# Optimization experiments

Hardware: AMD Instinct MI355X
Metric: run time of the kernel (lower is better)

Reference implementation:

```python
import jax, jax.numpy as jnp
import numpy as np

B, T, D = 2, 4096, 768
H = 12
HD = D // H  # 64
SCALE = 1.0 / np.sqrt(HD)


def setup_inputs() -> dict:
    key = jax.random.key(0)
    k1, k2, k3 = jax.random.split(key, 3)
    x = jax.random.normal(k1, (B, T, D), dtype=jnp.float32)
    W_qkv = jax.random.normal(k2, (D, 3 * D), dtype=jnp.float32) * (1.0 / np.sqrt(D))
    b_qkv = jnp.zeros((3 * D,), dtype=jnp.float32)
    W_out = jax.random.normal(k3, (D, D), dtype=jnp.float32) * (1.0 / np.sqrt(D))
    b_out = jnp.zeros((D,), dtype=jnp.float32)
    return {"x": x, "W_qkv": W_qkv, "b_qkv": b_qkv, "W_out": W_out, "b_out": b_out}


def reference(x, W_qkv, b_qkv, W_out, b_out):
    Bx, Tx, C = x.shape
    qkv = x @ W_qkv + b_qkv                                  # [B,T,3D]
    qkv = qkv.reshape(Bx, Tx, 3, H, HD).transpose(2, 0, 3, 1, 4)  # [3,B,H,T,hd]
    q, k, v = qkv[0], qkv[1], qkv[2]
    scores = jnp.einsum('bhqd,bhkd->bhqk', q, k) * SCALE      # [B,H,T,T]
    causal = jnp.tril(jnp.ones((Tx, Tx), dtype=bool))
    scores = jnp.where(causal[None, None], scores, -jnp.inf)
    attn = jax.nn.softmax(scores, axis=-1)
    out = jnp.einsum('bhqk,bhkd->bhqd', attn, v)              # [B,H,T,hd]
    out = out.transpose(0, 2, 1, 3).reshape(Bx, Tx, C)        # [B,T,D]
    return out @ W_out + b_out
```

## Files before the change

### kernel.cpp

```cpp
#include <hip/hip_runtime.h>
#include <cstdint>
#include <cstddef>

typedef _Float16 f16x8 __attribute__((ext_vector_type(8)));
typedef _Float16 f16x4 __attribute__((ext_vector_type(4)));
typedef float    f32x4 __attribute__((ext_vector_type(4)));

#define AS_GLOBAL __attribute__((address_space(1)))
#define AS_LDS    __attribute__((address_space(3)))

__device__ __forceinline__ void load16_to_lds(const _Float16* g, _Float16* l) {
    __builtin_amdgcn_global_load_lds((const AS_GLOBAL void*)g, (AS_LDS void*)l, 16, 0, 0);
}

#define BB   2
#define TT   4096
#define DD   768
#define NH   12
#define HDIM 64
#define D3   2304
#define SC2  (0.125f * 1.44269504088896f)

__global__ void cast_f32_f16(const float* __restrict__ in, _Float16* __restrict__ out, int n) {
    int i = (blockIdx.x * blockDim.x + threadIdx.x) * 4;
    float4 v = *(const float4*)(in + i);
    f16x4 h;
    h[0] = (_Float16)v.x; h[1] = (_Float16)v.y;
    h[2] = (_Float16)v.z; h[3] = (_Float16)v.w;
    *(f16x4*)(out + i) = h;
}

__global__ void transpose_cast(const float* __restrict__ in, _Float16* __restrict__ out,
                               int R, int C) {
    __shared__ float tile[32][33];
    const int bx = blockIdx.x * 32, by = blockIdx.y * 32;
    const int tx = threadIdx.x, ty = threadIdx.y;
#pragma unroll
    for (int j = 0; j < 32; j += 8)
        tile[ty + j][tx] = in[(size_t)(by + ty + j) * C + bx + tx];
    __syncthreads();
#pragma unroll
    for (int j = 0; j < 32; j += 8)
        out[(size_t)(bx + ty + j) * R + by + tx] = (_Float16)tile[tx][ty + j];
}

template <typename OutT, bool BIAS_ROW>
__global__ __launch_bounds__(256) void gemm_bt(const _Float16* __restrict__ A,
                                               const _Float16* __restrict__ Bt,
                                               const float* __restrict__ bias,
                                               OutT* __restrict__ C,
                                               int M, int N, int K) {
    __shared__ __align__(16) _Float16 As[128 * 32];
    __shared__ __align__(16) _Float16 Bs[128 * 32];
    const int tid  = threadIdx.x;
    const int wave = tid >> 6, lane = tid & 63, quad = lane >> 4, l16 = lane & 15;
    const int m0 = blockIdx.y * 128, n0 = blockIdx.x * 128;
    const int wm = (wave & 1) * 64, wn = (wave >> 1) * 64;
    const int rowc = lane >> 2, part = lane & 3;

    f32x4 acc[4][4];
#pragma unroll
    for (int i = 0; i < 4; ++i)
#pragma unroll
        for (int n = 0; n < 4; ++n) acc[i][n] = f32x4{0.f, 0.f, 0.f, 0.f};

    for (int k0 = 0; k0 < K; k0 += 32) {
        __syncthreads();
#pragma unroll
        for (int cc = 0; cc < 2; ++cc) {
            const int ch = wave * 2 + cc;
            load16_to_lds(A  + (size_t)(m0 + ch * 16 + rowc) * K + k0 + part * 8,
                          As + ch * 512);
            load16_to_lds(Bt + (size_t)(n0 + ch * 16 + rowc) * K + k0 + part * 8,
                          Bs + ch * 512);
        }
        __syncthreads();
#pragma unroll
        for (int i = 0; i < 4; ++i) {
            f16x8 a = *(const f16x8*)(As + (wm + i * 16 + l16) * 32 + quad * 8);
#pragma unroll
            for (int n = 0; n < 4; ++n) {
                f16x8 b = *(const f16x8*)(Bs + (wn + n * 16 + l16) * 32 + quad * 8);
                acc[i][n] = __builtin_amdgcn_mfma_f32_16x16x32_f16(a, b, acc[i][n], 0, 0, 0);
            }
        }
    }
#pragma unroll
    for (int i = 0; i < 4; ++i)
#pragma unroll
        for (int n = 0; n < 4; ++n)
#pragma unroll
            for (int r = 0; r < 4; ++r) {
                const int row = m0 + wm + i * 16 + quad * 4 + r;
                const int col = n0 + wn + n * 16 + l16;
                const float bv = BIAS_ROW ? bias[row] : bias[col];
                C[(size_t)row * N + col] = (OutT)(acc[i][n][r] + bv);
            }
}

__global__ __launch_bounds__(256) void attn_kernel(const _Float16* __restrict__ qk,
                                                   const _Float16* __restrict__ vt,
                                                   _Float16* __restrict__ ao) {
    __shared__ __align__(16) _Float16 Ks[2][64 * 64];
    __shared__ __align__(16) _Float16 Vs[2][80 * 64];
    __shared__ __align__(16) _Float16 Ps[4][16 * 80];
    const int b = blockIdx.z, h = blockIdx.y;
    const int tid = threadIdx.x;
    const int wave = tid >> 6, lane = tid & 63, quad = lane >> 4, l16 = lane & 15;

    if (tid < 16) {
        f16x8 ones;
#pragma unroll
        for (int j = 0; j < 8; ++j) ones[j] = (_Float16)1.0f;
        *(f16x8*)(Vs[tid >> 3] + 64 * 64 + (tid & 7) * 8) = ones;
    }

    const _Float16* pK[2];
    const _Float16* pV[2];
#pragma unroll
    for (int p = 0; p < 2; ++p) {
        const int j  = wave * 16 + p * 8 + (lane >> 3);
        const int sig = (j & 15) * 4 + (j >> 4);
        const int cdk = (lane & 7) ^ (j & 7);
        pK[p] = qk + (size_t)(b * TT + sig) * 1536 + DD + h * HDIM + cdk * 8;
        pV[p] = vt + (size_t)(h * HDIM + j) * 8192 + b * TT + cdk * 8;
    }
    auto stage = [&](int buf, int k0) {
#pragma unroll
        for (int p = 0; p < 2; ++p) {
            load16_to_lds(pK[p] + (size_t)k0 * 1536, Ks[buf] + (wave * 16 + p * 8) * 64);
            load16_to_lds(pV[p] + k0,                Vs[buf] + (wave * 16 + p * 8) * 64);
        }
    };

    _Float16* pw[4];
#pragma unroll
    for (int r = 0; r < 4; ++r) {
        const int row = quad * 4 + r;
        pw[r] = Ps[wave] + row * 80 + (((l16 >> 1) ^ (row & 7)) * 8) + (l16 & 1) * 4;
    }
    const _Float16* pr[2];
#pragma unroll
    for (int kh = 0; kh < 2; ++kh)
        pr[kh] = Ps[wave] + l16 * 80 + (((kh * 4 + quad) ^ (l16 & 7)) * 8);

    auto process = [&](int qt) {
        const int q0 = qt * 64;
        const int nkt = qt + 1;
        const int qrow = q0 + wave * 16 + quad * 4;
        f16x8 aq[2];
        {
            const int q = q0 + wave * 16 + l16;
            const _Float16* qp = qk + (size_t)(b * TT + q) * 1536 + h * HDIM + quad * 8;
            const _Float16 sc = (_Float16)SC2;
            aq[0] = *(const f16x8*)qp * sc;
            aq[1] = *(const f16x8*)(qp + 32) * sc;
        }
        f32x4 o[5];
#pragma unroll
        for (int n = 0; n < 5; ++n) o[n] = f32x4{0.f, 0.f, 0.f, 0.f};

        __syncthreads();
        stage(0, 0);
        int cur = 0;
        for (int kt = 0; kt < nkt; ++kt) {
            __syncthreads();
            if (kt + 1 < nkt) stage(cur ^ 1, (kt + 1) * 64);

            f32x4 s[4];
#pragma unroll
            for (int n = 0; n < 4; ++n) s[n] = f32x4{0.f, 0.f, 0.f, 0.f};
#pragma unroll
            for (int kh = 0; kh < 2; ++kh)
#pragma unroll
                for (int n = 0; n < 4; ++n) {
                    const int pos = (kh * 4 + quad) ^ (l16 & 7);
                    f16x8 bk = *(const f16x8*)(Ks[cur] + (n * 16 + l16) * 64 + pos * 8);
                    s[n] = __builtin_amdgcn_mfma_f32_16x16x32_f16(aq[kh], bk, s[n], 0, 0, 0);
                }

            if (kt == nkt - 1) {
#pragma unroll
                for (int n = 0; n < 4; ++n) {
                    const int kg = kt * 64 + l16 * 4 + n;
#pragma unroll
                    for (int r = 0; r < 4; ++r)
                        if (kg > qrow + r) s[n][r] = -1e30f;
                }
            }

#pragma unroll
            for (int r = 0; r < 4; ++r) {
                f16x4 pk;
#pragma unroll
                for (int n = 0; n < 4; ++n)
                    pk[n] = (_Float16)__builtin_amdgcn_exp2f(s[n][r]);
                *(f16x4*)pw[r] = pk;
            }

#pragma unroll
            for (int kh = 0; kh < 2; ++kh) {
                f16x8 ap = *(const f16x8*)pr[kh];
#pragma unroll
                for (int n = 0; n < 5; ++n) {
                    const int posv = (kh * 4 + quad) ^ (l16 & 7);
                    f16x8 bv = *(const f16x8*)(Vs[cur] + (n * 16 + l16) * 64 + posv * 8);
                    o[n] = __builtin_amdgcn_mfma_f32_16x16x32_f16(ap, bv, o[n], 0, 0, 0);
                }
            }
            cur ^= 1;
        }

#pragma unroll
        for (int r = 0; r < 4; ++r) {
            const float lr = __shfl(o[4][r], lane & 48);
            const float inv = 1.0f / lr;
            const int q = qrow + r;
#pragma unroll
            for (int n = 0; n < 4; ++n) {
                const int col = h * HDIM + n * 16 + l16;
                ao[(size_t)(b * TT + q) * DD + col] = (_Float16)(o[n][r] * inv);
            }
        }
    };

    process(63 - blockIdx.x);
    process(blockIdx.x);
}

extern "C" void kernel_launch(void* const* d_in, const int* in_sizes, int n_in,
                              void* d_out, int out_size, void* d_ws, size_t ws_size,
                              hipStream_t stream) {
    const float* x     = (const float*)d_in[0];
    const float* Wqkv  = (const float*)d_in[1];
    const float* bqkv  = (const float*)d_in[2];
    const float* Wout  = (const float*)d_in[3];
    const float* bout  = (const float*)d_in[4];
    float* out = (float*)d_out;

    char* ws = (char*)d_ws;
    _Float16* Xh    = (_Float16*)ws;  ws += (size_t)BB * TT * DD * 2;
    _Float16* Wqkvt = (_Float16*)ws;  ws += (size_t)D3 * DD * 2;
    _Float16* Wot   = (_Float16*)ws;  ws += (size_t)DD * DD * 2;
    _Float16* QKh   = (_Float16*)ws;  ws += (size_t)BB * TT * 1536 * 2;
    _Float16* VtG   = (_Float16*)ws;  ws += (size_t)DD * BB * TT * 2;
    _Float16* AOh   = (_Float16*)ws;  ws += (size_t)BB * TT * DD * 2;

    const int M = BB * TT;

    cast_f32_f16<<<(M * DD) / (256 * 4), 256, 0, stream>>>(x, Xh, M * DD);
    transpose_cast<<<dim3(D3 / 32, DD / 32), dim3(32, 8), 0, stream>>>(Wqkv, Wqkvt, DD, D3);
    transpose_cast<<<dim3(DD / 32, DD / 32), dim3(32, 8), 0, stream>>>(Wout, Wot, DD, DD);

    gemm_bt<_Float16, false><<<dim3(1536 / 128, M / 128), 256, 0, stream>>>(
        Xh, Wqkvt, bqkv, QKh, M, 1536, DD);
    gemm_bt<_Float16, true><<<dim3(M / 128, DD / 128), 256, 0, stream>>>(
        Wqkvt + (size_t)1536 * DD, Xh, bqkv + 1536, VtG, DD, M, DD);

    attn_kernel<<<dim3(32, NH, BB), 256, 0, stream>>>(QKh, VtG, AOh);

    gemm_bt<float, false><<<dim3(DD / 128, M / 128), 256, 0, stream>>>(
        AOh, Wot, bout, out, M, DD, DD);
}
```

Before: 260.3 us.

## Merge prep and QKV GEMM launches; restructure attention to 2 waves × 32 rows

The three cast/transpose kernels are merged into one prep launch, and the QK and V projection GEMMs become a single launch, which cuts launch overhead and lets the two GEMMs share the GPU. The attention kernel now runs 128 threads, with each wave owning 32 query rows. Each loaded K/V fragment feeds two MFMAs, raising reuse. The row sum is now taken by a separate MFMA against a ones vector instead of a padded V column. Risks are higher register pressure and fewer waves per block to hide latency.

```diff
diff --git a/kernel.cpp b/kernel.cpp
--- a/kernel.cpp
+++ b/kernel.cpp
@@ -21,20 +21,35 @@
 #define D3   2304
 #define SC2  (0.125f * 1.44269504088896f)
 
-__global__ void cast_f32_f16(const float* __restrict__ in, _Float16* __restrict__ out, int n) {
-    int i = (blockIdx.x * blockDim.x + threadIdx.x) * 4;
-    float4 v = *(const float4*)(in + i);
-    f16x4 h;
-    h[0] = (_Float16)v.x; h[1] = (_Float16)v.y;
-    h[2] = (_Float16)v.z; h[3] = (_Float16)v.w;
-    *(f16x4*)(out + i) = h;
-}
-
-__global__ void transpose_cast(const float* __restrict__ in, _Float16* __restrict__ out,
-                               int R, int C) {
+__global__ __launch_bounds__(256) void prep(const float* __restrict__ x,
+                                            _Float16* __restrict__ Xh,
+                                            const float* __restrict__ Wqkv,
+                                            _Float16* __restrict__ Wqkvt,
+                                            const float* __restrict__ Wout,
+                                            _Float16* __restrict__ Wot) {
+    const int bid = blockIdx.x, tid = threadIdx.x;
+    if (bid < 6144) {
+        const int i = bid * 1024 + tid * 4;
+        float4 v = *(const float4*)(x + i);
+        f16x4 h;
+        h[0] = (_Float16)v.x; h[1] = (_Float16)v.y;
+        h[2] = (_Float16)v.z; h[3] = (_Float16)v.w;
+        *(f16x4*)(Xh + i) = h;
+        return;
+    }
     __shared__ float tile[32][33];
-    const int bx = blockIdx.x * 32, by = blockIdx.y * 32;
-    const int tx = threadIdx.x, ty = threadIdx.y;
+    const float* in; _Float16* out; int C, bx, by;
+    if (bid < 7872) {
+        const int t = bid - 6144;
+        in = Wqkv; out = Wqkvt; C = 2304;
+        bx = (t % 72) * 32; by = (t / 72) * 32;
+    } else {
+        const int t = bid - 7872;
+        in = Wout; out = Wot; C = 768;
+        bx = (t % 24) * 32; by = (t / 24) * 32;
+    }
+    const int R = 768;
+    const int tx = tid & 31, ty = tid >> 5;
 #pragma unroll
     for (int j = 0; j < 32; j += 8)
         tile[ty + j][tx] = in[(size_t)(by + ty + j) * C + bx + tx];
@@ -44,17 +59,15 @@
         out[(size_t)(bx + ty + j) * R + by + tx] = (_Float16)tile[tx][ty + j];
 }
 
-template <typename OutT, bool BIAS_ROW>
-__global__ __launch_bounds__(256) void gemm_bt(const _Float16* __restrict__ A,
-                                               const _Float16* __restrict__ Bt,
-                                               const float* __restrict__ bias,
-                                               OutT* __restrict__ C,
-                                               int M, int N, int K) {
-    __shared__ __align__(16) _Float16 As[128 * 32];
-    __shared__ __align__(16) _Float16 Bs[128 * 32];
+template <typename OutT>
+__device__ __forceinline__ void gemm_body(const _Float16* __restrict__ A,
+                                          const _Float16* __restrict__ Bt,
+                                          const float* __restrict__ bias, bool bias_row,
+                                          OutT* __restrict__ C, int N, int K,
+                                          int m0, int n0,
+                                          _Float16* As, _Float16* Bs) {
     const int tid  = threadIdx.x;
     const int wave = tid >> 6, lane = tid & 63, quad = lane >> 4, l16 = lane & 15;
-    const int m0 = blockIdx.y * 128, n0 = blockIdx.x * 128;
     const int wm = (wave & 1) * 64, wn = (wave >> 1) * 64;
     const int rowc = lane >> 2, part = lane & 3;
 
@@ -93,33 +106,60 @@
             for (int r = 0; r < 4; ++r) {
                 const int row = m0 + wm + i * 16 + quad * 4 + r;
                 const int col = n0 + wn + n * 16 + l16;
-                const float bv = BIAS_ROW ? bias[row] : bias[col];
+                const float bv = bias_row ? bias[row] : bias[col];
                 C[(size_t)row * N + col] = (OutT)(acc[i][n][r] + bv);
             }
 }
 
-__global__ __launch_bounds__(256) void attn_kernel(const _Float16* __restrict__ qk,
+__global__ __launch_bounds__(256) void gemm_qkv(const _Float16* __restrict__ Xh,
+                                                const _Float16* __restrict__ Wqkvt,
+                                                const float* __restrict__ bqkv,
+                                                _Float16* __restrict__ QKh,
+                                                _Float16* __restrict__ VtG) {
+    __shared__ __align__(16) _Float16 As[128 * 32];
+    __shared__ __align__(16) _Float16 Bs[128 * 32];
+    const int bid = blockIdx.x;
+    if (bid < 768) {
+        const int bx = bid % 12, by = bid / 12;
+        gemm_body<_Float16>(Xh, Wqkvt, bqkv, false, QKh, 1536, DD,
+                            by * 128, bx * 128, As, Bs);
+    } else {
+        const int t = bid - 768;
+        const int bx = t % 64, by = t / 64;
+        gemm_body<_Float16>(Wqkvt + (size_t)1536 * DD, Xh, bqkv + 1536, true, VtG,
+                            8192, DD, by * 128, bx * 128, As, Bs);
+    }
+}
+
+__global__ __launch_bounds__(256) void gemm_out(const _Float16* __restrict__ A,
+                                                const _Float16* __restrict__ Bt,
+                                                const float* __restrict__ bias,
+                                                float* __restrict__ C) {
+    __shared__ __align__(16) _Float16 As[128 * 32];
+    __shared__ __align__(16) _Float16 Bs[128 * 32];
+    gemm_body<float>(A, Bt, bias, false, C, DD, DD,
+                     (int)blockIdx.y * 128, (int)blockIdx.x * 128, As, Bs);
+}
+
+__global__ __launch_bounds__(128) void attn_kernel(const _Float16* __restrict__ qk,
                                                    const _Float16* __restrict__ vt,
                                                    _Float16* __restrict__ ao) {
     __shared__ __align__(16) _Float16 Ks[2][64 * 64];
-    __shared__ __align__(16) _Float16 Vs[2][80 * 64];
-    __shared__ __align__(16) _Float16 Ps[4][16 * 80];
+    __shared__ __align__(16) _Float16 Vs[2][64 * 64];
+    __shared__ __align__(16) _Float16 Ps[2][32 * 64];
     const int b = blockIdx.z, h = blockIdx.y;
     const int tid = threadIdx.x;
     const int wave = tid >> 6, lane = tid & 63, quad = lane >> 4, l16 = lane & 15;
 
-    if (tid < 16) {
-        f16x8 ones;
-#pragma unroll
-        for (int j = 0; j < 8; ++j) ones[j] = (_Float16)1.0f;
-        *(f16x8*)(Vs[tid >> 3] + 64 * 64 + (tid & 7) * 8) = ones;
-    }
-
-    const _Float16* pK[2];
-    const _Float16* pV[2];
-#pragma unroll
-    for (int p = 0; p < 2; ++p) {
-        const int j  = wave * 16 + p * 8 + (lane >> 3);
+    f16x8 ones;
+#pragma unroll
+    for (int j = 0; j < 8; ++j) ones[j] = (_Float16)1.0f;
+
+    const _Float16* pK[4];
+    const _Float16* pV[4];
+#pragma unroll
+    for (int p = 0; p < 4; ++p) {
+        const int j  = wave * 32 + p * 8 + (lane >> 3);
         const int sig = (j & 15) * 4 + (j >> 4);
         const int cdk = (lane & 7) ^ (j & 7);
         pK[p] = qk + (size_t)(b * TT + sig) * 1536 + DD + h * HDIM + cdk * 8;
@@ -127,38 +167,48 @@
     }
     auto stage = [&](int buf, int k0) {
 #pragma unroll
-        for (int p = 0; p < 2; ++p) {
-            load16_to_lds(pK[p] + (size_t)k0 * 1536, Ks[buf] + (wave * 16 + p * 8) * 64);
-            load16_to_lds(pV[p] + k0,                Vs[buf] + (wave * 16 + p * 8) * 64);
+        for (int p = 0; p < 4; ++p) {
+            load16_to_lds(pK[p] + (size_t)k0 * 1536, Ks[buf] + (wave * 32 + p * 8) * 64);
+            load16_to_lds(pV[p] + k0,                Vs[buf] + (wave * 32 + p * 8) * 64);
         }
     };
 
-    _Float16* pw[4];
-#pragma unroll
-    for (int r = 0; r < 4; ++r) {
-        const int row = quad * 4 + r;
-        pw[r] = Ps[wave] + row * 80 + (((l16 >> 1) ^ (row & 7)) * 8) + (l16 & 1) * 4;
-    }
-    const _Float16* pr[2];
-#pragma unroll
-    for (int kh = 0; kh < 2; ++kh)
-        pr[kh] = Ps[wave] + l16 * 80 + (((kh * 4 + quad) ^ (l16 & 7)) * 8);
+    _Float16* pw[2][4];
+#pragma unroll
+    for (int mi = 0; mi < 2; ++mi)
+#pragma unroll
+        for (int r = 0; r < 4; ++r) {
+            const int row = mi * 16 + quad * 4 + r;
+            pw[mi][r] = Ps[wave] + row * 64 + (((l16 >> 1) ^ (row & 7)) * 8) + (l16 & 1) * 4;
+        }
+    const _Float16* pr[2][2];
+#pragma unroll
+    for (int mi = 0; mi < 2; ++mi)
+#pragma unroll
+        for (int kh = 0; kh < 2; ++kh) {
+            const int row = mi * 16 + l16;
+            pr[mi][kh] = Ps[wave] + row * 64 + (((kh * 4 + quad) ^ (row & 7)) * 8);
+        }
 
     auto process = [&](int qt) {
         const int q0 = qt * 64;
         const int nkt = qt + 1;
-        const int qrow = q0 + wave * 16 + quad * 4;
-        f16x8 aq[2];
-        {
-            const int q = q0 + wave * 16 + l16;
+        f16x8 aq[2][2];
+#pragma unroll
+        for (int mi = 0; mi < 2; ++mi) {
+            const int q = q0 + wave * 32 + mi * 16 + l16;
             const _Float16* qp = qk + (size_t)(b * TT + q) * 1536 + h * HDIM + quad * 8;
             const _Float16 sc = (_Float16)SC2;
-            aq[0] = *(const f16x8*)qp * sc;
-            aq[1] = *(const f16x8*)(qp + 32) * sc;
-        }
-        f32x4 o[5];
-#pragma unroll
-        for (int n = 0; n < 5; ++n) o[n] = f32x4{0.f, 0.f, 0.f, 0.f};
+            aq[mi][0] = *(const f16x8*)qp * sc;
+            aq[mi][1] = *(const f16x8*)(qp + 32) * sc;
+        }
+        f32x4 o[2][4], lac[2];
+#pragma unroll
+        for (int mi = 0; mi < 2; ++mi) {
+#pragma unroll
+            for (int n = 0; n < 4; ++n) o[mi][n] = f32x4{0.f, 0.f, 0.f, 0.f};
+            lac[mi] = f32x4{0.f, 0.f, 0.f, 0.f};
+        }
 
         __syncthreads();
         stage(0, 0);
@@ -167,16 +217,21 @@
             __syncthreads();
             if (kt + 1 < nkt) stage(cur ^ 1, (kt + 1) * 64);
 
-            f32x4 s[4];
-#pragma unroll
-            for (int n = 0; n < 4; ++n) s[n] = f32x4{0.f, 0.f, 0.f, 0.f};
+            f32x4 s[2][4];
+#pragma unroll
+            for (int mi = 0; mi < 2; ++mi)
+#pragma unroll
+                for (int n = 0; n < 4; ++n) s[mi][n] = f32x4{0.f, 0.f, 0.f, 0.f};
 #pragma unroll
             for (int kh = 0; kh < 2; ++kh)
 #pragma unroll
                 for (int n = 0; n < 4; ++n) {
                     const int pos = (kh * 4 + quad) ^ (l16 & 7);
                     f16x8 bk = *(const f16x8*)(Ks[cur] + (n * 16 + l16) * 64 + pos * 8);
-                    s[n] = __builtin_amdgcn_mfma_f32_16x16x32_f16(aq[kh], bk, s[n], 0, 0, 0);
+#pragma unroll
+                    for (int mi = 0; mi < 2; ++mi)
+                        s[mi][n] = __builtin_amdgcn_mfma_f32_16x16x32_f16(aq[mi][kh], bk,
+                                                                          s[mi][n], 0, 0, 0);
                 }
 
             if (kt == nkt - 1) {
@@ -184,44 +239,60 @@
                 for (int n = 0; n < 4; ++n) {
                     const int kg = kt * 64 + l16 * 4 + n;
 #pragma unroll
-                    for (int r = 0; r < 4; ++r)
-                        if (kg > qrow + r) s[n][r] = -1e30f;
-                }
-            }
-
-#pragma unroll
-            for (int r = 0; r < 4; ++r) {
-                f16x4 pk;
-#pragma unroll
-                for (int n = 0; n < 4; ++n)
-                    pk[n] = (_Float16)__builtin_amdgcn_exp2f(s[n][r]);
-                *(f16x4*)pw[r] = pk;
-            }
+                    for (int mi = 0; mi < 2; ++mi) {
+                        const int qg = q0 + wave * 32 + mi * 16 + quad * 4;
+#pragma unroll
+                        for (int r = 0; r < 4; ++r)
+                            if (kg > qg + r) s[mi][n][r] = -1e30f;
+                    }
+                }
+            }
+
+#pragma unroll
+            for (int mi = 0; mi < 2; ++mi)
+#pragma unroll
+                for (int r = 0; r < 4; ++r) {
+                    f16x4 pk;
+#pragma unroll
+                    for (int n = 0; n < 4; ++n)
+                        pk[n] = (_Float16)__builtin_amdgcn_exp2f(s[mi][n][r]);
+                    *(f16x4*)pw[mi][r] = pk;
+                }
 
 #pragma unroll
             for (int kh = 0; kh < 2; ++kh) {
-                f16x8 ap = *(const f16x8*)pr[kh];
-#pragma unroll
-                for (int n = 0; n < 5; ++n) {
+                f16x8 ap[2];
+#pragma unroll
+                for (int mi = 0; mi < 2; ++mi) {
+                    ap[mi] = *(const f16x8*)pr[mi][kh];
+                    lac[mi] = __builtin_amdgcn_mfma_f32_16x16x32_f16(ap[mi], ones,
+                                                                     lac[mi], 0, 0, 0);
+                }
+#pragma unroll
+                for (int n = 0; n < 4; ++n) {
                     const int posv = (kh * 4 + quad) ^ (l16 & 7);
                     f16x8 bv = *(const f16x8*)(Vs[cur] + (n * 16 + l16) * 64 + posv * 8);
-                    o[n] = __builtin_amdgcn_mfma_f32_16x16x32_f16(ap, bv, o[n], 0, 0, 0);
+#pragma unroll
+                    for (int mi = 0; mi < 2; ++mi)
+                        o[mi][n] = __builtin_amdgcn_mfma_f32_16x16x32_f16(ap[mi], bv,
+                                                                          o[mi][n], 0, 0, 0);
                 }
             }
             cur ^= 1;
         }
 
 #pragma unroll
-        for (int r = 0; r < 4; ++r) {
-            const float lr = __shfl(o[4][r], lane & 48);
-            const float inv = 1.0f / lr;
-            const int q = qrow + r;
-#pragma unroll
-            for (int n = 0; n < 4; ++n) {
-                const int col = h * HDIM + n * 16 + l16;
-                ao[(size_t)(b * TT + q) * DD + col] = (_Float16)(o[n][r] * inv);
-            }
-        }
+        for (int mi = 0; mi < 2; ++mi)
+#pragma unroll
+            for (int r = 0; r < 4; ++r) {
+                const float inv = 1.0f / lac[mi][r];
+                const int q = q0 + wave * 32 + mi * 16 + quad * 4 + r;
+#pragma unroll
+                for (int n = 0; n < 4; ++n) {
+                    const int col = h * HDIM + n * 16 + l16;
+                    ao[(size_t)(b * TT + q) * DD + col] = (_Float16)(o[mi][n][r] * inv);
+                }
+            }
     };
 
     process(63 - blockIdx.x);
@@ -246,19 +317,11 @@
     _Float16* VtG   = (_Float16*)ws;  ws += (size_t)DD * BB * TT * 2;
     _Float16* AOh   = (_Float16*)ws;  ws += (size_t)BB * TT * DD * 2;
 
-    const int M = BB * TT;
-
-    cast_f32_f16<<<(M * DD) / (256 * 4), 256, 0, stream>>>(x, Xh, M * DD);
-    transpose_cast<<<dim3(D3 / 32, DD / 32), dim3(32, 8), 0, stream>>>(Wqkv, Wqkvt, DD, D3);
-    transpose_cast<<<dim3(DD / 32, DD / 32), dim3(32, 8), 0, stream>>>(Wout, Wot, DD, DD);
-
-    gemm_bt<_Float16, false><<<dim3(1536 / 128, M / 128), 256, 0, stream>>>(
-        Xh, Wqkvt, bqkv, QKh, M, 1536, DD);
-    gemm_bt<_Float16, true><<<dim3(M / 128, DD / 128), 256, 0, stream>>>(
-        Wqkvt + (size_t)1536 * DD, Xh, bqkv + 1536, VtG, DD, M, DD);
-
-    attn_kernel<<<dim3(32, NH, BB), 256, 0, stream>>>(QKh, VtG, AOh);
-
-    gemm_bt<float, false><<<dim3(DD / 128, M / 128), 256, 0, stream>>>(
-        AOh, Wot, bout, out, M, DD, DD);
-}
+    prep<<<8448, 256, 0, stream>>>(x, Xh, Wqkv, Wqkvt, Wout, Wot);
+
+    gemm_qkv<<<1152, 256, 0, stream>>>(Xh, Wqkvt, bqkv, QKh, VtG);
+
+    attn_kernel<<<dim3(32, NH, BB), 128, 0, stream>>>(QKh, VtG, AOh);
+
+    gemm_out<<<dim3(DD / 128, (BB * TT) / 128), 256, 0, stream>>>(AOh, Wot, bout, out);
+}
```

New measurement: 259.9 us. No clear change (-0.1%).

## Fuse prep and QKV launches, widen GEMM K-tile, one q-tile per attention block

Applied to the files above, without the earlier changes.

Combines the cast and the two transpose kernels into one launch, and the Q/K and V^T GEMMs into one launch. Doubles the GEMM K step to 64 to halve the barrier count. Attention now processes one query tile per block over a doubled grid instead of pairing heavy and light tiles. The softmax denominator is now computed with an MFMA against a ones vector, dropping the extra LDS column. This risks load imbalance from the causal triangle and uses more LDS per GEMM block.

```diff
diff --git a/kernel.cpp b/kernel.cpp
--- a/kernel.cpp
+++ b/kernel.cpp
@@ -21,20 +21,35 @@
 #define D3   2304
 #define SC2  (0.125f * 1.44269504088896f)
 
-__global__ void cast_f32_f16(const float* __restrict__ in, _Float16* __restrict__ out, int n) {
-    int i = (blockIdx.x * blockDim.x + threadIdx.x) * 4;
-    float4 v = *(const float4*)(in + i);
-    f16x4 h;
-    h[0] = (_Float16)v.x; h[1] = (_Float16)v.y;
-    h[2] = (_Float16)v.z; h[3] = (_Float16)v.w;
-    *(f16x4*)(out + i) = h;
-}
-
-__global__ void transpose_cast(const float* __restrict__ in, _Float16* __restrict__ out,
-                               int R, int C) {
+__global__ __launch_bounds__(256) void prep(const float* __restrict__ x,
+                                            _Float16* __restrict__ Xh,
+                                            const float* __restrict__ Wqkv,
+                                            _Float16* __restrict__ Wqkvt,
+                                            const float* __restrict__ Wout,
+                                            _Float16* __restrict__ Wot) {
+    const int bid = blockIdx.x, tid = threadIdx.x;
+    if (bid < 6144) {
+        const int i = bid * 1024 + tid * 4;
+        float4 v = *(const float4*)(x + i);
+        f16x4 h;
+        h[0] = (_Float16)v.x; h[1] = (_Float16)v.y;
+        h[2] = (_Float16)v.z; h[3] = (_Float16)v.w;
+        *(f16x4*)(Xh + i) = h;
+        return;
+    }
     __shared__ float tile[32][33];
-    const int bx = blockIdx.x * 32, by = blockIdx.y * 32;
-    const int tx = threadIdx.x, ty = threadIdx.y;
+    const float* in; _Float16* out; int C, bx, by;
+    if (bid < 7872) {
+        const int t = bid - 6144;
+        in = Wqkv; out = Wqkvt; C = 2304;
+        bx = (t % 72) * 32; by = (t / 72) * 32;
+    } else {
+        const int t = bid - 7872;
+        in = Wout; out = Wot; C = 768;
+        bx = (t % 24) * 32; by = (t / 24) * 32;
+    }
+    const int R = 768;
+    const int tx = tid & 31, ty = tid >> 5;
 #pragma unroll
     for (int j = 0; j < 32; j += 8)
         tile[ty + j][tx] = in[(size_t)(by + ty + j) * C + bx + tx];
@@ -44,19 +59,17 @@
         out[(size_t)(bx + ty + j) * R + by + tx] = (_Float16)tile[tx][ty + j];
 }
 
-template <typename OutT, bool BIAS_ROW>
-__global__ __launch_bounds__(256) void gemm_bt(const _Float16* __restrict__ A,
-                                               const _Float16* __restrict__ Bt,
-                                               const float* __restrict__ bias,
-                                               OutT* __restrict__ C,
-                                               int M, int N, int K) {
-    __shared__ __align__(16) _Float16 As[128 * 32];
-    __shared__ __align__(16) _Float16 Bs[128 * 32];
+template <typename OutT>
+__device__ __forceinline__ void gemm_body(const _Float16* __restrict__ A,
+                                          const _Float16* __restrict__ Bt,
+                                          const float* __restrict__ bias, bool bias_row,
+                                          OutT* __restrict__ C, int N, int K,
+                                          int m0, int n0,
+                                          _Float16* As, _Float16* Bs) {
     const int tid  = threadIdx.x;
     const int wave = tid >> 6, lane = tid & 63, quad = lane >> 4, l16 = lane & 15;
-    const int m0 = blockIdx.y * 128, n0 = blockIdx.x * 128;
     const int wm = (wave & 1) * 64, wn = (wave >> 1) * 64;
-    const int rowc = lane >> 2, part = lane & 3;
+    const int rowc = lane >> 3, part = lane & 7;
 
     f32x4 acc[4][4];
 #pragma unroll
@@ -64,24 +77,27 @@
 #pragma unroll
         for (int n = 0; n < 4; ++n) acc[i][n] = f32x4{0.f, 0.f, 0.f, 0.f};
 
-    for (int k0 = 0; k0 < K; k0 += 32) {
+    for (int k0 = 0; k0 < K; k0 += 64) {
         __syncthreads();
 #pragma unroll
-        for (int cc = 0; cc < 2; ++cc) {
-            const int ch = wave * 2 + cc;
-            load16_to_lds(A  + (size_t)(m0 + ch * 16 + rowc) * K + k0 + part * 8,
+        for (int cc = 0; cc < 4; ++cc) {
+            const int ch = wave * 4 + cc;
+            load16_to_lds(A  + (size_t)(m0 + ch * 8 + rowc) * K + k0 + part * 8,
                           As + ch * 512);
-            load16_to_lds(Bt + (size_t)(n0 + ch * 16 + rowc) * K + k0 + part * 8,
+            load16_to_lds(Bt + (size_t)(n0 + ch * 8 + rowc) * K + k0 + part * 8,
                           Bs + ch * 512);
         }
         __syncthreads();
 #pragma unroll
         for (int i = 0; i < 4; ++i) {
-            f16x8 a = *(const f16x8*)(As + (wm + i * 16 + l16) * 32 + quad * 8);
-#pragma unroll
-            for (int n = 0; n < 4; ++n) {
-                f16x8 b = *(const f16x8*)(Bs + (wn + n * 16 + l16) * 32 + quad * 8);
-                acc[i][n] = __builtin_amdgcn_mfma_f32_16x16x32_f16(a, b, acc[i][n], 0, 0, 0);
+            f16x8 a0 = *(const f16x8*)(As + (wm + i * 16 + l16) * 64 + quad * 8);
+            f16x8 a1 = *(const f16x8*)(As + (wm + i * 16 + l16) * 64 + 32 + quad * 8);
+#pragma unroll
+            for (int n = 0; n < 4; ++n) {
+                f16x8 b0 = *(const f16x8*)(Bs + (wn + n * 16 + l16) * 64 + quad * 8);
+                f16x8 b1 = *(const f16x8*)(Bs + (wn + n * 16 + l16) * 64 + 32 + quad * 8);
+                acc[i][n] = __builtin_amdgcn_mfma_f32_16x16x32_f16(a0, b0, acc[i][n], 0, 0, 0);
+                acc[i][n] = __builtin_amdgcn_mfma_f32_16x16x32_f16(a1, b1, acc[i][n], 0, 0, 0);
             }
         }
     }
@@ -93,27 +109,55 @@
             for (int r = 0; r < 4; ++r) {
                 const int row = m0 + wm + i * 16 + quad * 4 + r;
                 const int col = n0 + wn + n * 16 + l16;
-                const float bv = BIAS_ROW ? bias[row] : bias[col];
+                const float bv = bias_row ? bias[row] : bias[col];
                 C[(size_t)row * N + col] = (OutT)(acc[i][n][r] + bv);
             }
+}
+
+__global__ __launch_bounds__(256) void gemm_qkv(const _Float16* __restrict__ Xh,
+                                                const _Float16* __restrict__ Wqkvt,
+                                                const float* __restrict__ bqkv,
+                                                _Float16* __restrict__ QKh,
+                                                _Float16* __restrict__ VtG) {
+    __shared__ __align__(16) _Float16 As[128 * 64];
+    __shared__ __align__(16) _Float16 Bs[128 * 64];
+    const int bid = blockIdx.x;
+    if (bid < 768) {
+        const int bx = bid % 12, by = bid / 12;
+        gemm_body<_Float16>(Xh, Wqkvt, bqkv, false, QKh, 1536, DD,
+                            by * 128, bx * 128, As, Bs);
+    } else {
+        const int t = bid - 768;
+        const int bx = t % 64, by = t / 64;
+        gemm_body<_Float16>(Wqkvt + (size_t)1536 * DD, Xh, bqkv + 1536, true, VtG,
+                            8192, DD, by * 128, bx * 128, As, Bs);
+    }
+}
+
+__global__ __launch_bounds__(256) void gemm_out(const _Float16* __restrict__ A,
+                                                const _Float16* __restrict__ Bt,
+                                                const float* __restrict__ bias,
+                                                float* __restrict__ C) {
+    __shared__ __align__(16) _Float16 As[128 * 64];
+    __shared__ __align__(16) _Float16 Bs[128 * 64];
+    gemm_body<float>(A, Bt, bias, false, C, DD, DD,
+                     (int)blockIdx.y * 128, (int)blockIdx.x * 128, As, Bs);
 }
 
 __global__ __launch_bounds__(256) void attn_kernel(const _Float16* __restrict__ qk,
                                                    const _Float16* __restrict__ vt,
                                                    _Float16* __restrict__ ao) {
     __shared__ __align__(16) _Float16 Ks[2][64 * 64];
-    __shared__ __align__(16) _Float16 Vs[2][80 * 64];
-    __shared__ __align__(16) _Float16 Ps[4][16 * 80];
+    __shared__ __align__(16) _Float16 Vs[2][64 * 64];
+    __shared__ __align__(16) _Float16 Ps[4][16 * 64];
     const int b = blockIdx.z, h = blockIdx.y;
+    const int qt = 63 - blockIdx.x;
     const int tid = threadIdx.x;
     const int wave = tid >> 6, lane = tid & 63, quad = lane >> 4, l16 = lane & 15;
 
-    if (tid < 16) {
-        f16x8 ones;
-#pragma unroll
-        for (int j = 0; j < 8; ++j) ones[j] = (_Float16)1.0f;
-        *(f16x8*)(Vs[tid >> 3] + 64 * 64 + (tid & 7) * 8) = ones;
-    }
+    f16x8 ones;
+#pragma unroll
+    for (int j = 0; j < 8; ++j) ones[j] = (_Float16)1.0f;
 
     const _Float16* pK[2];
     const _Float16* pV[2];
@@ -137,95 +181,90 @@
 #pragma unroll
     for (int r = 0; r < 4; ++r) {
         const int row = quad * 4 + r;
-        pw[r] = Ps[wave] + row * 80 + (((l16 >> 1) ^ (row & 7)) * 8) + (l16 & 1) * 4;
+        pw[r] = Ps[wave] + row * 64 + (((l16 >> 1) ^ (row & 7)) * 8) + (l16 & 1) * 4;
     }
     const _Float16* pr[2];
 #pragma unroll
     for (int kh = 0; kh < 2; ++kh)
-        pr[kh] = Ps[wave] + l16 * 80 + (((kh * 4 + quad) ^ (l16 & 7)) * 8);
-
-    auto process = [&](int qt) {
-        const int q0 = qt * 64;
-        const int nkt = qt + 1;
-        const int qrow = q0 + wave * 16 + quad * 4;
-        f16x8 aq[2];
-        {
-            const int q = q0 + wave * 16 + l16;
-            const _Float16* qp = qk + (size_t)(b * TT + q) * 1536 + h * HDIM + quad * 8;
-            const _Float16 sc = (_Float16)SC2;
-            aq[0] = *(const f16x8*)qp * sc;
-            aq[1] = *(const f16x8*)(qp + 32) * sc;
-        }
-        f32x4 o[5];
-#pragma unroll
-        for (int n = 0; n < 5; ++n) o[n] = f32x4{0.f, 0.f, 0.f, 0.f};
-
+        pr[kh] = Ps[wave] + l16 * 64 + (((kh * 4 + quad) ^ (l16 & 7)) * 8);
+
+    const int q0 = qt * 64;
+    const int nkt = qt + 1;
+    const int qrow = q0 + wave * 16 + quad * 4;
+    f16x8 aq[2];
+    {
+        const int q = q0 + wave * 16 + l16;
+        const _Float16* qp = qk + (size_t)(b * TT + q) * 1536 + h * HDIM + quad * 8;
+        const _Float16 sc = (_Float16)SC2;
+        aq[0] = *(const f16x8*)qp * sc;
+        aq[1] = *(const f16x8*)(qp + 32) * sc;
+    }
+    f32x4 o[4], lac;
+#pragma unroll
+    for (int n = 0; n < 4; ++n) o[n] = f32x4{0.f, 0.f, 0.f, 0.f};
+    lac = f32x4{0.f, 0.f, 0.f, 0.f};
+
+    stage(0, 0);
+    int cur = 0;
+    for (int kt = 0; kt < nkt; ++kt) {
         __syncthreads();
-        stage(0, 0);
-        int cur = 0;
-        for (int kt = 0; kt < nkt; ++kt) {
-            __syncthreads();
-            if (kt + 1 < nkt) stage(cur ^ 1, (kt + 1) * 64);
-
-            f32x4 s[4];
-#pragma unroll
-            for (int n = 0; n < 4; ++n) s[n] = f32x4{0.f, 0.f, 0.f, 0.f};
-#pragma unroll
-            for (int kh = 0; kh < 2; ++kh)
-#pragma unroll
-                for (int n = 0; n < 4; ++n) {
-                    const int pos = (kh * 4 + quad) ^ (l16 & 7);
-                    f16x8 bk = *(const f16x8*)(Ks[cur] + (n * 16 + l16) * 64 + pos * 8);
-                    s[n] = __builtin_amdgcn_mfma_f32_16x16x32_f16(aq[kh], bk, s[n], 0, 0, 0);
-                }
-
-            if (kt == nkt - 1) {
-#pragma unroll
-                for (int n = 0; n < 4; ++n) {
-                    const int kg = kt * 64 + l16 * 4 + n;
-#pragma unroll
-                    for (int r = 0; r < 4; ++r)
-                        if (kg > qrow + r) s[n][r] = -1e30f;
-                }
-            }
-
-#pragma unroll
-            for (int r = 0; r < 4; ++r) {
-                f16x4 pk;
-#pragma unroll
-                for (int n = 0; n < 4; ++n)
-                    pk[n] = (_Float16)__builtin_amdgcn_exp2f(s[n][r]);
-                *(f16x4*)pw[r] = pk;
-            }
-
-#pragma unroll
-            for (int kh = 0; kh < 2; ++kh) {
-                f16x8 ap = *(const f16x8*)pr[kh];
-#pragma unroll
-                for (int n = 0; n < 5; ++n) {
-                    const int posv = (kh * 4 + quad) ^ (l16 & 7);
-                    f16x8 bv = *(const f16x8*)(Vs[cur] + (n * 16 + l16) * 64 + posv * 8);
-                    o[n] = __builtin_amdgcn_mfma_f32_16x16x32_f16(ap, bv, o[n], 0, 0, 0);
-                }
-            }
-            cur ^= 1;
+        if (kt + 1 < nkt) stage(cur ^ 1, (kt + 1) * 64);
+
+        f32x4 s[4];
+#pragma unroll
+        for (int n = 0; n < 4; ++n) s[n] = f32x4{0.f, 0.f, 0.f, 0.f};
+#pragma unroll
+        for (int kh = 0; kh < 2; ++kh)
+#pragma unroll
+            for (int n = 0; n < 4; ++n) {
+                const int pos = (kh * 4 + quad) ^ (l16 & 7);
+                f16x8 bk = *(const f16x8*)(Ks[cur] + (n * 16 + l16) * 64 + pos * 8);
+                s[n] = __builtin_amdgcn_mfma_f32_16x16x32_f16(aq[kh], bk, s[n], 0, 0, 0);
+            }
+
+        if (kt == nkt - 1) {
+#pragma unroll
+            for (int n = 0; n < 4; ++n) {
+                const int kg = kt * 64 + l16 * 4 + n;
+#pragma unroll
+                for (int r = 0; r < 4; ++r)
+                    if (kg > qrow + r) s[n][r] = -1e30f;
+            }
         }
 
 #pragma unroll
         for (int r = 0; r < 4; ++r) {
-            const float lr = __shfl(o[4][r], lane & 48);
-            const float inv = 1.0f / lr;
-            const int q = qrow + r;
-#pragma unroll
-            for (int n = 0; n < 4; ++n) {
-                const int col = h * HDIM + n * 16 + l16;
-                ao[(size_t)(b * TT + q) * DD + col] = (_Float16)(o[n][r] * inv);
-            }
-        }
-    };
-
-    process(63 - blockIdx.x);
-    process(blockIdx.x);
+            f16x4 pk;
+#pragma unroll
+            for (int n = 0; n < 4; ++n)
+                pk[n] = (_Float16)__builtin_amdgcn_exp2f(s[n][r]);
+            *(f16x4*)pw[r] = pk;
+        }
+
+#pragma unroll
+        for (int kh = 0; kh < 2; ++kh) {
+            f16x8 ap = *(const f16x8*)pr[kh];
+            lac = __builtin_amdgcn_mfma_f32_16x16x32_f16(ap, ones, lac, 0, 0, 0);
+#pragma unroll
+            for (int n = 0; n < 4; ++n) {
+                const int posv = (kh * 4 + quad) ^ (l16 & 7);
+                f16x8 bv = *(const f16x8*)(Vs[cur] + (n * 16 + l16) * 64 + posv * 8);
+                o[n] = __builtin_amdgcn_mfma_f32_16x16x32_f16(ap, bv, o[n], 0, 0, 0);
+            }
+        }
+        cur ^= 1;
+    }
+
+#pragma unroll
+    for (int r = 0; r < 4; ++r) {
+        const float inv = 1.0f / lac[r];
+        const int q = qrow + r;
+#pragma unroll
+        for (int n = 0; n < 4; ++n) {
+            const int col = h * HDIM + n * 16 + l16;
+            ao[(size_t)(b * TT + q) * DD + col] = (_Float16)(o[n][r] * inv);
+        }
+    }
 }
 
 extern "C" void kernel_launch(void* const* d_in, const int* in_sizes, int n_in,
@@ -246,19 +285,11 @@
     _Float16* VtG   = (_Float16*)ws;  ws += (size_t)DD * BB * TT * 2;
     _Float16* AOh   = (_Float16*)ws;  ws += (size_t)BB * TT * DD * 2;
 
-    const int M = BB * TT;
-
-    cast_f32_f16<<<(M * DD) / (256 * 4), 256, 0, stream>>>(x, Xh, M * DD);
-    transpose_cast<<<dim3(D3 / 32, DD / 32), dim3(32, 8), 0, stream>>>(Wqkv, Wqkvt, DD, D3);
-    transpose_cast<<<dim3(DD / 32, DD / 32), dim3(32, 8), 0, stream>>>(Wout, Wot, DD, DD);
-
-    gemm_bt<_Float16, false><<<dim3(1536 / 128, M / 128), 256, 0, stream>>>(
-        Xh, Wqkvt, bqkv, QKh, M, 1536, DD);
-    gemm_bt<_Float16, true><<<dim3(M / 128, DD / 128), 256, 0, stream>>>(
-        Wqkvt + (size_t)1536 * DD, Xh, bqkv + 1536, VtG, DD, M, DD);
-
-    attn_kernel<<<dim3(32, NH, BB), 256, 0, stream>>>(QKh, VtG, AOh);
-
-    gemm_bt<float, false><<<dim3(DD / 128, M / 128), 256, 0, stream>>>(
-        AOh, Wot, bout, out, M, DD, DD);
-}
+    prep<<<8448, 256, 0, stream>>>(x, Xh, Wqkv, Wqkvt, Wout, Wot);
+
+    gemm_qkv<<<1152, 256, 0, stream>>>(Xh, Wqkvt, bqkv, QKh, VtG);
+
+    attn_kernel<<<dim3(64, NH, BB), 256, 0, stream>>>(QKh, VtG, AOh);
+
+    gemm_out<<<dim3(DD / 128, (BB * TT) / 128), 256, 0, stream>>>(AOh, Wot, bout, out);
+}
```

Measured after the change: 291.7 us. +12.1%, slower.
